# Kernel optimization log

Hardware: AMD Instinct MI355X
Metric: run time of the kernel (lower is better)

## Reference

```python
import jax, jax.numpy as jnp
import numpy as np

B, N, DIM = 16, 1024, 512
H, KD, D = 16, 32, 128          # num_heads, key_dim, d = attn_ratio*key_dim
DH = H * D                      # 2048
HQKV = DH + 2 * H * KD          # 3072
RES = 32
SCALE = KD ** -0.5
EPS = 1e-5


def _make_bias_idxs():
    ii = np.arange(N)
    px, py = ii // RES, ii % RES
    dx = np.abs(px[:, None] - px[None, :])
    dy = np.abs(py[:, None] - py[None, :])
    return (dx * RES + dy).astype(np.int32)  # (N, N), values in [0, RES*RES)


def setup_inputs() -> dict:
    key = jax.random.key(0)
    ks = jax.random.split(key, 6)
    return {
        "x": jax.random.normal(ks[0], (B, N, DIM), jnp.float32),
        "gamma": jnp.ones((DIM,), jnp.float32),
        "beta": jnp.zeros((DIM,), jnp.float32),
        "qkv_w": jax.random.normal(ks[1], (HQKV, DIM), jnp.float32) * 0.02,
        "qkv_b": jax.random.normal(ks[2], (HQKV,), jnp.float32) * 0.02,
        "proj_w": jax.random.normal(ks[3], (DIM, DH), jnp.float32) * 0.02,
        "proj_b": jax.random.normal(ks[4], (DIM,), jnp.float32) * 0.02,
        "attention_biases": jax.random.normal(ks[5], (H, RES * RES), jnp.float32) * 0.02,
        "bias_idxs": jnp.asarray(_make_bias_idxs()),
    }


def reference(x, gamma, beta, qkv_w, qkv_b, proj_w, proj_b, attention_biases, bias_idxs):
    # LayerNorm
    mu = jnp.mean(x, axis=-1, keepdims=True)
    var = jnp.mean(jnp.square(x - mu), axis=-1, keepdims=True)
    xn = (x - mu) * jax.lax.rsqrt(var + EPS) * gamma + beta
    # QKV projection -> (B, H, N, kd+kd+d)
    qkv = (xn @ qkv_w.T + qkv_b).reshape(B, N, H, 2 * KD + D).transpose(0, 2, 1, 3)
    q, k, v = qkv[..., :KD], qkv[..., KD:2 * KD], qkv[..., 2 * KD:]
    # Relative-position bias gather: (H, N, N)
    bias = attention_biases[:, bias_idxs]
    attn = jnp.einsum("bhnk,bhmk->bhnm", q, k) * SCALE + bias
    attn = jax.nn.softmax(attn, axis=-1)
    out = jnp.einsum("bhnm,bhmd->bhnd", attn, v)  # (B, H, N, D)
    out = out.transpose(0, 2, 1, 3).reshape(B, N, DH)
    return out @ proj_w.T + proj_b
```

## Files before the change

kernel.cpp:

```cpp
#include <hip/hip_runtime.h>

#define DIM_   512
#define NSEQ   1024
#define BB     16
#define HH     16
#define KD_    32
#define DD_    128
#define LDQKV  3072
#define DH_    2048
#define SCALE_ 0.17677669529663687f

typedef __bf16 bf16x8 __attribute__((ext_vector_type(8)));
typedef float  f32x4  __attribute__((ext_vector_type(4)));

typedef __attribute__((address_space(1))) const unsigned int guint;
typedef __attribute__((address_space(3))) unsigned int luint;
#define GLL16(gp, lp) __builtin_amdgcn_global_load_lds((guint*)(gp), (luint*)(lp), 16, 0, 0)

static __device__ __forceinline__ unsigned short f2bf(float f) {
  unsigned int u = __builtin_bit_cast(unsigned int, f);
  u += 0x7fffu + ((u >> 16) & 1u);
  return (unsigned short)(u >> 16);
}
#define SGM(t) ((((t) & 3) << 1) | (((t) >> 2) & 1))

__global__ __launch_bounds__(256) void cvt_kernel(const float* __restrict__ in,
                                                  unsigned short* __restrict__ out,
                                                  int n) {
  int i = blockIdx.x * 256 + threadIdx.x;
  if (i < n) out[i] = f2bf(in[i]);
}

__global__ __launch_bounds__(256) void ln_kernel(const float* __restrict__ x,
                                                 const float* __restrict__ gamma,
                                                 const float* __restrict__ beta,
                                                 unsigned short* __restrict__ xn) {
  int row = blockIdx.x, t = threadIdx.x;
  const float* xr = x + (size_t)row * DIM_;
  float2 v = *(const float2*)(xr + t * 2);
  float s = v.x + v.y, sq = v.x * v.x + v.y * v.y;
#pragma unroll
  for (int off = 32; off; off >>= 1) {
    s  += __shfl_xor(s, off, 64);
    sq += __shfl_xor(sq, off, 64);
  }
  __shared__ float red[8];
  int wid = t >> 6, lane = t & 63;
  if (lane == 0) { red[wid * 2] = s; red[wid * 2 + 1] = sq; }
  __syncthreads();
  float S  = red[0] + red[2] + red[4] + red[6];
  float SQ = red[1] + red[3] + red[5] + red[7];
  float mu   = S * (1.f / DIM_);
  float var  = SQ * (1.f / DIM_) - mu * mu;
  float rstd = rsqrtf(var + 1e-5f);
  int c = t * 2;
  xn[(size_t)row * DIM_ + c]     = f2bf((v.x - mu) * rstd * gamma[c]     + beta[c]);
  xn[(size_t)row * DIM_ + c + 1] = f2bf((v.y - mu) * rstd * gamma[c + 1] + beta[c + 1]);
}

template <typename OUT>
__global__ __launch_bounds__(256) void gemm_gll(const unsigned short* __restrict__ A, int lda,
                                                const unsigned short* __restrict__ W, int ldb,
                                                const float* __restrict__ bias,
                                                OUT* __restrict__ C, int ldc,
                                                int K) {
  __shared__ unsigned short a_sm[128][64];
  __shared__ unsigned short b_sm[128][64];
  int tid = threadIdx.x;
  int lane = tid & 63, w = tid >> 6;
  int quad = lane >> 4, l15 = lane & 15;
  int wr = w >> 1, wc = w & 1;
  long tm = (long)blockIdx.y * 128, tn = (long)blockIdx.x * 128;
  int srow = w * 8 + (lane >> 3), scol = (lane & 7) * 8;

  f32x4 acc[4][4] = {};

  for (int k0 = 0; k0 < K; k0 += 64) {
    __syncthreads();
#pragma unroll
    for (int it = 0; it < 4; it++) {
      GLL16(A + (tm + it * 32 + srow) * lda + k0 + scol, &a_sm[it * 32 + w * 8][0]);
      GLL16(W + (tn + it * 32 + srow) * ldb + k0 + scol, &b_sm[it * 32 + w * 8][0]);
    }
    __syncthreads();
#pragma unroll
    for (int kk = 0; kk < 64; kk += 32) {
      bf16x8 af[4], bfr[4];
#pragma unroll
      for (int i = 0; i < 4; i++)
        af[i] = *(const bf16x8*)&a_sm[wr * 64 + i * 16 + l15][kk + quad * 8];
#pragma unroll
      for (int j = 0; j < 4; j++)
        bfr[j] = *(const bf16x8*)&b_sm[wc * 64 + j * 16 + l15][kk + quad * 8];
#pragma unroll
      for (int i = 0; i < 4; i++)
#pragma unroll
        for (int j = 0; j < 4; j++)
          acc[i][j] = __builtin_amdgcn_mfma_f32_16x16x32_bf16(af[i], bfr[j], acc[i][j], 0, 0, 0);
    }
  }
#pragma unroll
  for (int j = 0; j < 4; j++) {
    long col = tn + wc * 64 + j * 16 + l15;
    float bv = bias[col];
#pragma unroll
    for (int i = 0; i < 4; i++) {
      long row0 = tm + wr * 64 + i * 16 + quad * 4;
#pragma unroll
      for (int r = 0; r < 4; r++) {
        float val = acc[i][j][r] + bv;
        if constexpr (__is_same(OUT, float))
          C[(row0 + r) * ldc + col] = val;
        else
          C[(row0 + r) * ldc + col] = f2bf(val);
      }
    }
  }
}

__global__ __launch_bounds__(256) void attn_kernel(const unsigned short* __restrict__ qkv,
                                                   const float* __restrict__ ab,
                                                   unsigned short* __restrict__ attn_out) {
  __shared__ float lut[1024];
  __shared__ unsigned short vt[128][72];
  __shared__ unsigned short k_sm[64][40];
  __shared__ unsigned short p_sm[4][16][72];
  __shared__ float l_sm[64];

  int tid = threadIdx.x;
  int lane = tid & 63, w = tid >> 6;
  int quad = lane >> 4, l15 = lane & 15;
  int wq = w & 1, wd = w >> 1;
  int qb = blockIdx.x;
  int bh = blockIdx.y;
  int b = bh >> 4, h = bh & 15;
  const unsigned short* base = qkv + (size_t)b * NSEQ * LDQKV + h * 192;

  for (int t = tid; t < 1024; t += 256) lut[t] = ab[h * 1024 + t];

  int qr = qb * 64 + w * 16 + l15;
  bf16x8 qf = *(const bf16x8*)(base + (size_t)qr * LDQKV + quad * 8);

  f32x4 accO[2][4] = {};
  float l_r[4] = {0.f, 0.f, 0.f, 0.f};

  int pcol_lo = (l15 & 8) | SGM(l15 & 7);
  int kkey = tid >> 2, kch = tid & 3;

  uint4 vreg[4];
  uint4 kreg;
#pragma unroll
  for (int i = 0; i < 4; i++) {
    int c = tid + i * 256;
    int m = c >> 4, c8 = c & 15;
    vreg[i] = *(const uint4*)(base + (size_t)m * LDQKV + 64 + c8 * 8);
  }
  kreg = *(const uint4*)(base + (size_t)kkey * LDQKV + 32 + kch * 8);

  for (int kt = 0; kt < 16; kt++) {
    __syncthreads();
#pragma unroll
    for (int i = 0; i < 4; i++) {
      int c = tid + i * 256;
      int m = c >> 4, c8 = c & 15;
      const unsigned short* pv = (const unsigned short*)&vreg[i];
      int col = (((m >> 3) ^ (c8 & 7)) << 3) | SGM(m & 7);
#pragma unroll
      for (int e = 0; e < 8; e++) vt[c8 * 8 + e][col] = pv[e];
    }
    *(uint4*)&k_sm[kkey][kch * 8] = kreg;
    __syncthreads();

    if (kt < 15) {
#pragma unroll
      for (int i = 0; i < 4; i++) {
        int c = tid + i * 256;
        int m = c >> 4, c8 = c & 15;
        vreg[i] = *(const uint4*)(base + (size_t)((kt + 1) * 64 + m) * LDQKV + 64 + c8 * 8);
      }
      kreg = *(const uint4*)(base + (size_t)((kt + 1) * 64 + kkey) * LDQKV + 32 + kch * 8);
    }

    f32x4 s[4];
#pragma unroll
    for (int nb = 0; nb < 4; nb++) {
      bf16x8 kf = *(const bf16x8*)&k_sm[nb * 16 + l15][quad * 8];
      f32x4 z = {};
      s[nb] = __builtin_amdgcn_mfma_f32_16x16x32_bf16(qf, kf, z, 0, 0, 0);
    }

#pragma unroll
    for (int nb = 0; nb < 4; nb++) {
      int cc = kt * 64 + nb * 16 + l15;
      int cx = cc >> 5, cy = cc & 31;
#pragma unroll
      for (int r = 0; r < 4; r++) {
        int rr = qb * 64 + w * 16 + quad * 4 + r;
        int dx = (rr >> 5) - cx; dx = dx < 0 ? -dx : dx;
        int dy = (rr & 31) - cy; dy = dy < 0 ? -dy : dy;
        float p = __expf(fmaf(s[nb][r], SCALE_, lut[dx * 32 + dy]));
        l_r[r] += p;
        p_sm[w][quad * 4 + r][nb * 16 + pcol_lo] = f2bf(p);
      }
    }
    __syncthreads();

#pragma unroll
    for (int kc = 0; kc < 2; kc++) {
      bf16x8 pf[2];
#pragma unroll
      for (int g = 0; g < 2; g++)
        pf[g] = *(const bf16x8*)&p_sm[wq * 2 + g][l15][kc * 32 + quad * 8];
#pragma unroll
      for (int j = 0; j < 4; j++) {
        int db = wd * 4 + j;
        int f = (db * 2 + (l15 >> 3)) & 7;
        int colb = ((kc * 4 + quad) ^ f) << 3;
        bf16x8 vf = *(const bf16x8*)&vt[db * 16 + l15][colb];
#pragma unroll
        for (int g = 0; g < 2; g++)
          accO[g][j] = __builtin_amdgcn_mfma_f32_16x16x32_bf16(pf[g], vf, accO[g][j], 0, 0, 0);
      }
    }
  }
#pragma unroll
  for (int r = 0; r < 4; r++) {
#pragma unroll
    for (int off = 8; off; off >>= 1) l_r[r] += __shfl_xor(l_r[r], off, 16);
  }
  if (l15 == 0) {
#pragma unroll
    for (int r = 0; r < 4; r++) l_sm[w * 16 + quad * 4 + r] = l_r[r];
  }
  __syncthreads();
#pragma unroll
  for (int g = 0; g < 2; g++) {
#pragma unroll
    for (int r = 0; r < 4; r++) {
      int row16 = (wq * 2 + g) * 16 + quad * 4 + r;
      float inv = 1.f / l_sm[row16];
      int row = qb * 64 + row16;
      size_t obase = ((size_t)b * NSEQ + row) * DH_ + h * DD_;
#pragma unroll
      for (int j = 0; j < 4; j++)
        attn_out[obase + (wd * 4 + j) * 16 + l15] = f2bf(accO[g][j][r] * inv);
    }
  }
}

extern "C" void kernel_launch(void* const* d_in, const int* in_sizes, int n_in,
                              void* d_out, int out_size, void* d_ws, size_t ws_size,
                              hipStream_t stream) {
  const float* x      = (const float*)d_in[0];
  const float* gamma  = (const float*)d_in[1];
  const float* beta   = (const float*)d_in[2];
  const float* qkv_w  = (const float*)d_in[3];
  const float* qkv_b  = (const float*)d_in[4];
  const float* proj_w = (const float*)d_in[5];
  const float* proj_b = (const float*)d_in[6];
  const float* ab     = (const float*)d_in[7];

  char* ws = (char*)d_ws;
  unsigned short* xn      = (unsigned short*)(ws);
  unsigned short* wqkv    = (unsigned short*)(ws + (size_t)16 * 1048576);
  unsigned short* wproj   = (unsigned short*)(ws + (size_t)19 * 1048576);
  unsigned short* qkv     = (unsigned short*)(ws + (size_t)21 * 1048576);
  unsigned short* attnout = (unsigned short*)(ws + (size_t)117 * 1048576);
  float* out = (float*)d_out;

  cvt_kernel<<<dim3(6144), dim3(256), 0, stream>>>(qkv_w, wqkv, 3072 * 512);
  cvt_kernel<<<dim3(4096), dim3(256), 0, stream>>>(proj_w, wproj, 512 * 2048);
  ln_kernel<<<dim3(16384), dim3(256), 0, stream>>>(x, gamma, beta, xn);
  gemm_gll<unsigned short><<<dim3(24, 128), dim3(256), 0, stream>>>(xn, 512, wqkv, 512, qkv_b, qkv, 3072, 512);
  attn_kernel<<<dim3(16, 256), dim3(256), 0, stream>>>(qkv, ab, attnout);
  gemm_gll<float><<<dim3(4, 128), dim3(256), 0, stream>>>(attnout, 2048, wproj, 2048, proj_b, out, 512, 2048);
}
```

Before: 446.3 us.

## Keep attention probabilities in registers via transposed QK MFMA and bpermute

The attention kernel now computes S transposed (K as the A operand), so each wave owns all 64 keys for its 16 query rows and can feed P to the PV MFMA through ds_bpermute register shuffles instead of a shared-memory p_sm buffer. This removes one __syncthreads per tile and the final l_sm reduction. Each wave now computes all 128 output columns for its own 16 rows, rather than sharing a 2x2 split across waves. Bias index math is partly precomputed (dy per lane, dx per tile), and the grid is remapped to a 1D launch that groups consecutive blocks over neighbouring heads and query blocks. The cost is 8 bpermutes per k-chunk, more accumulator registers, and extra vt LDS reads per wave.

New measurement: 491.2 us. +10.1%, slower.

```diff
diff --git a/kernel.cpp b/kernel.cpp
--- a/kernel.cpp
+++ b/kernel.cpp
@@ -12,6 +12,7 @@
 
 typedef __bf16 bf16x8 __attribute__((ext_vector_type(8)));
 typedef float  f32x4  __attribute__((ext_vector_type(4)));
+typedef unsigned int u32x4v __attribute__((ext_vector_type(4)));
 
 typedef __attribute__((address_space(1))) const unsigned int guint;
 typedef __attribute__((address_space(3))) unsigned int luint;
@@ -124,27 +125,37 @@
   __shared__ float lut[1024];
   __shared__ unsigned short vt[128][72];
   __shared__ unsigned short k_sm[64][40];
-  __shared__ unsigned short p_sm[4][16][72];
-  __shared__ float l_sm[64];
 
   int tid = threadIdx.x;
   int lane = tid & 63, w = tid >> 6;
   int quad = lane >> 4, l15 = lane & 15;
-  int wq = w & 1, wd = w >> 1;
-  int qb = blockIdx.x;
-  int bh = blockIdx.y;
+
+  int id = blockIdx.x;
+  int bh = ((id >> 7) << 3) | (id & 7);
+  int qb = (id >> 3) & 15;
   int b = bh >> 4, h = bh & 15;
   const unsigned short* base = qkv + (size_t)b * NSEQ * LDQKV + h * 192;
 
   for (int t = tid; t < 1024; t += 256) lut[t] = ab[h * 1024 + t];
 
-  int qr = qb * 64 + w * 16 + l15;
-  bf16x8 qf = *(const bf16x8*)(base + (size_t)qr * LDQKV + quad * 8);
-
-  f32x4 accO[2][4] = {};
-  float l_r[4] = {0.f, 0.f, 0.f, 0.f};
-
-  int pcol_lo = (l15 & 8) | SGM(l15 & 7);
+  int qg = qb * 64 + w * 16 + l15;
+  bf16x8 qf = *(const bf16x8*)(base + (size_t)qg * LDQKV + quad * 8);
+
+  int rx = qg >> 5, ry = qg & 31;
+  int dy_pre[8];
+#pragma unroll
+  for (int i = 0; i < 8; i++) {
+    int cy = ((i >> 2) << 4) | (quad * 4 + (i & 3));
+    int d = ry - cy; dy_pre[i] = d < 0 ? -d : d;
+  }
+
+  int ixA = ((quad & 1) * 32 + l15) * 4;
+  int ixB = ixA + 64;
+  bool hiq = quad >= 2;
+
+  f32x4 accO[8] = {};
+  float l_r = 0.f;
+
   int kkey = tid >> 2, kch = tid & 3;
 
   uint4 vreg[4];
@@ -181,70 +192,78 @@
       kreg = *(const uint4*)(base + (size_t)((kt + 1) * 64 + kkey) * LDQKV + 32 + kch * 8);
     }
 
-    f32x4 s[4];
+    f32x4 st[4];
 #pragma unroll
     for (int nb = 0; nb < 4; nb++) {
       bf16x8 kf = *(const bf16x8*)&k_sm[nb * 16 + l15][quad * 8];
       f32x4 z = {};
-      s[nb] = __builtin_amdgcn_mfma_f32_16x16x32_bf16(qf, kf, z, 0, 0, 0);
-    }
-
+      st[nb] = __builtin_amdgcn_mfma_f32_16x16x32_bf16(kf, qf, z, 0, 0, 0);
+    }
+
+    int d0 = rx - 2 * kt;     int dxa = d0 < 0 ? -d0 : d0;
+    int d1 = d0 - 1;          int dxb = d1 < 0 ? -d1 : d1;
+    int lb0 = dxa << 5, lb1 = dxb << 5;
+
+    unsigned pk[8];
 #pragma unroll
     for (int nb = 0; nb < 4; nb++) {
-      int cc = kt * 64 + nb * 16 + l15;
-      int cx = cc >> 5, cy = cc & 31;
-#pragma unroll
-      for (int r = 0; r < 4; r++) {
-        int rr = qb * 64 + w * 16 + quad * 4 + r;
-        int dx = (rr >> 5) - cx; dx = dx < 0 ? -dx : dx;
-        int dy = (rr & 31) - cy; dy = dy < 0 ? -dy : dy;
-        float p = __expf(fmaf(s[nb][r], SCALE_, lut[dx * 32 + dy]));
-        l_r[r] += p;
-        p_sm[w][quad * 4 + r][nb * 16 + pcol_lo] = f2bf(p);
-      }
-    }
-    __syncthreads();
+      int lb = (nb & 2) ? lb1 : lb0;
+#pragma unroll
+      for (int t = 0; t < 2; t++) {
+        float p0 = __expf(fmaf(st[nb][2 * t],     SCALE_, lut[lb + dy_pre[(nb & 1) * 4 + 2 * t]]));
+        float p1 = __expf(fmaf(st[nb][2 * t + 1], SCALE_, lut[lb + dy_pre[(nb & 1) * 4 + 2 * t + 1]]));
+        l_r += p0 + p1;
+        unsigned short u0 = __builtin_bit_cast(unsigned short, (__bf16)p0);
+        unsigned short u1 = __builtin_bit_cast(unsigned short, (__bf16)p1);
+        pk[nb * 2 + t] = (unsigned)u0 | ((unsigned)u1 << 16);
+      }
+    }
 
 #pragma unroll
     for (int kc = 0; kc < 2; kc++) {
-      bf16x8 pf[2];
-#pragma unroll
-      for (int g = 0; g < 2; g++)
-        pf[g] = *(const bf16x8*)&p_sm[wq * 2 + g][l15][kc * 32 + quad * 8];
-#pragma unroll
-      for (int j = 0; j < 4; j++) {
-        int db = wd * 4 + j;
+      int s0 = (int)pk[4 * kc + 0], s1 = (int)pk[4 * kc + 1];
+      int s2 = (int)pk[4 * kc + 2], s3 = (int)pk[4 * kc + 3];
+      unsigned a0 = (unsigned)__builtin_amdgcn_ds_bpermute(ixA, s0);
+      unsigned a1 = (unsigned)__builtin_amdgcn_ds_bpermute(ixA, s1);
+      unsigned a2 = (unsigned)__builtin_amdgcn_ds_bpermute(ixA, s2);
+      unsigned a3 = (unsigned)__builtin_amdgcn_ds_bpermute(ixA, s3);
+      unsigned b0 = (unsigned)__builtin_amdgcn_ds_bpermute(ixB, s0);
+      unsigned b1 = (unsigned)__builtin_amdgcn_ds_bpermute(ixB, s1);
+      unsigned b2 = (unsigned)__builtin_amdgcn_ds_bpermute(ixB, s2);
+      unsigned b3 = (unsigned)__builtin_amdgcn_ds_bpermute(ixB, s3);
+      unsigned u0 = hiq ? a2 : a0;
+      unsigned u1 = hiq ? a3 : a1;
+      unsigned v0 = hiq ? b2 : b0;
+      unsigned v1 = hiq ? b3 : b1;
+      u32x4v paw;
+      paw.x = (u0 & 0xffffu) | (v0 << 16);
+      paw.y = (u0 >> 16)     | (v0 & 0xffff0000u);
+      paw.z = (u1 & 0xffffu) | (v1 << 16);
+      paw.w = (u1 >> 16)     | (v1 & 0xffff0000u);
+      bf16x8 paf = __builtin_bit_cast(bf16x8, paw);
+
+#pragma unroll
+      for (int db = 0; db < 8; db++) {
         int f = (db * 2 + (l15 >> 3)) & 7;
         int colb = ((kc * 4 + quad) ^ f) << 3;
         bf16x8 vf = *(const bf16x8*)&vt[db * 16 + l15][colb];
-#pragma unroll
-        for (int g = 0; g < 2; g++)
-          accO[g][j] = __builtin_amdgcn_mfma_f32_16x16x32_bf16(pf[g], vf, accO[g][j], 0, 0, 0);
-      }
-    }
-  }
+        accO[db] = __builtin_amdgcn_mfma_f32_16x16x32_bf16(paf, vf, accO[db], 0, 0, 0);
+      }
+    }
+  }
+
+  l_r += __shfl_xor(l_r, 16, 64);
+  l_r += __shfl_xor(l_r, 32, 64);
+
 #pragma unroll
   for (int r = 0; r < 4; r++) {
-#pragma unroll
-    for (int off = 8; off; off >>= 1) l_r[r] += __shfl_xor(l_r[r], off, 16);
-  }
-  if (l15 == 0) {
-#pragma unroll
-    for (int r = 0; r < 4; r++) l_sm[w * 16 + quad * 4 + r] = l_r[r];
-  }
-  __syncthreads();
-#pragma unroll
-  for (int g = 0; g < 2; g++) {
-#pragma unroll
-    for (int r = 0; r < 4; r++) {
-      int row16 = (wq * 2 + g) * 16 + quad * 4 + r;
-      float inv = 1.f / l_sm[row16];
-      int row = qb * 64 + row16;
-      size_t obase = ((size_t)b * NSEQ + row) * DH_ + h * DD_;
-#pragma unroll
-      for (int j = 0; j < 4; j++)
-        attn_out[obase + (wd * 4 + j) * 16 + l15] = f2bf(accO[g][j][r] * inv);
-    }
+    float lr = __shfl(l_r, quad * 4 + r, 16);
+    float inv = 1.f / lr;
+    int row = qb * 64 + w * 16 + quad * 4 + r;
+    size_t obase = ((size_t)b * NSEQ + row) * DH_ + h * DD_;
+#pragma unroll
+    for (int db = 0; db < 8; db++)
+      attn_out[obase + db * 16 + l15] = f2bf(accO[db][r] * inv);
   }
 }
 
@@ -272,6 +291,6 @@
   cvt_kernel<<<dim3(4096), dim3(256), 0, stream>>>(proj_w, wproj, 512 * 2048);
   ln_kernel<<<dim3(16384), dim3(256), 0, stream>>>(x, gamma, beta, xn);
   gemm_gll<unsigned short><<<dim3(24, 128), dim3(256), 0, stream>>>(xn, 512, wqkv, 512, qkv_b, qkv, 3072, 512);
-  attn_kernel<<<dim3(16, 256), dim3(256), 0, stream>>>(qkv, ab, attnout);
+  attn_kernel<<<dim3(4096), dim3(256), 0, stream>>>(qkv, ab, attnout);
   gemm_gll<float><<<dim3(4, 128), dim3(256), 0, stream>>>(attnout, 2048, wproj, 2048, proj_b, out, 512, 2048);
 }
```
